# Performance work log

Hardware: AMD Instinct MI355X
Metric: run time of the kernel (lower is better)

## Reference

```python
import jax, jax.numpy as jnp
import numpy as np

B, T, D, E, H = 4, 2048, 2048, 4, 8192  # H = 4*D
TOPK = 2
CAPACITY_FACTOR = 1


def setup_inputs() -> dict:
    key = jax.random.key(0)
    k0, k1, k2, k3 = jax.random.split(key, 4)
    x = jax.random.normal(k0, (B, T, D), dtype=jnp.float32)
    Wg = jax.random.normal(k1, (D, E), dtype=jnp.float32) * 0.02  # router gate weight
    bg = jnp.zeros((E,), dtype=jnp.float32)                        # router gate bias (nn.Linear default)
    W1 = jax.random.normal(k2, (E, D, H), dtype=jnp.float32) * (1.0 / np.sqrt(D))  # per-expert fc (no bias)
    W2 = jax.random.normal(k3, (E, H, D), dtype=jnp.float32) * (1.0 / np.sqrt(H))  # per-expert proj (no bias)
    return {"x": x, "Wg": Wg, "bg": bg, "W1": W1, "W2": W2}


def reference(x, Wg, bg, W1, W2):
    Bq, Tq, Dq = x.shape
    N = Bq * Tq
    capacity = int(N * CAPACITY_FACTOR / E)  # static python int

    flat_x = x.reshape(N, Dq)
    logits = flat_x @ Wg + bg                              # [N, E]
    top_vals, top_idx = jax.lax.top_k(logits, TOPK)        # [N, TOPK]
    sparse = jnp.full_like(logits, -jnp.inf)
    sparse = sparse.at[jnp.arange(N)[:, None], top_idx].set(top_vals)
    probs = jax.nn.softmax(sparse, axis=-1)                # zeros outside top-k

    out = jnp.zeros_like(flat_x)
    for i in range(E):  # small fixed expert count
        assigned = (top_idx == i).any(axis=-1)             # [N]
        score = jnp.where(assigned, probs[:, i], -jnp.inf)
        sel_p, sel_idx = jax.lax.top_k(score, capacity)    # capacity-limited, highest prob first
        p = jnp.where(jnp.isfinite(sel_p), sel_p, 0.0)[:, None]  # invalid slots contribute 0
        tok = flat_x[sel_idx]                              # [cap, D]
        h = jax.nn.gelu(tok @ W1[i], approximate=False)    # exact GELU like nn.GELU()
        y = (h @ W2[i]) * p                                # [cap, D]
        out = out.at[sel_idx].add(y)
    return out.reshape(Bq, Tq, Dq)
```

## Files before the change

kernel.cpp:

```cpp
#include <hip/hip_runtime.h>
#include <hip/hip_bf16.h>
#include <math.h>
#include <stdint.h>

#define N_TOK 8192
#define DMODEL 2048
#define NEXP 4
#define HDIM 8192
#define CAP 2048

typedef __attribute__((ext_vector_type(4))) float f32x4;
typedef __attribute__((ext_vector_type(8))) short s16x8;
typedef __attribute__((ext_vector_type(4))) unsigned short u16x4;

__device__ __forceinline__ unsigned short f2bf(float f) {
  __hip_bfloat16 h = __float2bfloat16(f);
  return __builtin_bit_cast(unsigned short, h);
}

__device__ __forceinline__ void gload_lds16(const void* g, void* l) {
  __builtin_amdgcn_global_load_lds(
      (const __attribute__((address_space(1))) unsigned int*)(uintptr_t)g,
      (__attribute__((address_space(3))) unsigned int*)(unsigned int)(uintptr_t)l,
      16, 0, 0);
}

__global__ __launch_bounds__(256) void router_kernel(
    const float* __restrict__ x, const float* __restrict__ Wg,
    const float* __restrict__ bg, float* __restrict__ probs) {
  int token = blockIdx.x * 4 + (threadIdx.x >> 6);
  int lane = threadIdx.x & 63;
  const float* xr = x + (size_t)token * DMODEL;
  double a0 = 0, a1 = 0, a2 = 0, a3 = 0;
  for (int i = lane; i < DMODEL; i += 64) {
    float xv = xr[i];
    float4 w = ((const float4*)Wg)[i];
    a0 += (double)xv * (double)w.x;
    a1 += (double)xv * (double)w.y;
    a2 += (double)xv * (double)w.z;
    a3 += (double)xv * (double)w.w;
  }
  for (int off = 32; off > 0; off >>= 1) {
    a0 += __shfl_down(a0, off);
    a1 += __shfl_down(a1, off);
    a2 += __shfl_down(a2, off);
    a3 += __shfl_down(a3, off);
  }
  if (lane == 0) {
    float l[4] = {(float)(a0 + (double)bg[0]), (float)(a1 + (double)bg[1]),
                  (float)(a2 + (double)bg[2]), (float)(a3 + (double)bg[3])};
    int e1 = 0;
    for (int e = 1; e < 4; ++e) if (l[e] > l[e1]) e1 = e;
    int e2 = (e1 == 0) ? 1 : 0;
    for (int e = e2 + 1; e < 4; ++e) { if (e == e1) continue; if (l[e] > l[e2]) e2 = e; }
    float d = l[e2] - l[e1];
    float ex = expf(d);
    float z = 1.0f + ex;
    float pr[4] = {0.f, 0.f, 0.f, 0.f};
    pr[e1] = 1.0f / z;
    pr[e2] = ex / z;
    float* pp = probs + (size_t)token * 4;
    pp[0] = pr[0]; pp[1] = pr[1]; pp[2] = pr[2]; pp[3] = pr[3];
  }
}

__global__ __launch_bounds__(256) void select_kernel(
    const float* __restrict__ probs, int* __restrict__ sel_idx, float* __restrict__ sel_p) {
  __shared__ unsigned long long keys[N_TOK];
  int e = blockIdx.x;
  for (int i = threadIdx.x; i < N_TOK; i += blockDim.x) {
    float p = probs[(size_t)i * 4 + e];
    unsigned hi = (p > 0.f) ? __float_as_uint(p) : 0u;
    keys[i] = ((unsigned long long)hi << 32) | (unsigned)(0xFFFFFFFFu - (unsigned)i);
  }
  __syncthreads();
  for (int k = 2; k <= N_TOK; k <<= 1) {
    for (int j = k >> 1; j > 0; j >>= 1) {
      for (int i = threadIdx.x; i < N_TOK; i += blockDim.x) {
        int ixj = i ^ j;
        if (ixj > i) {
          bool ddd = ((i & k) == 0);
          unsigned long long a = keys[i], b = keys[ixj];
          if ((a < b) == ddd) { keys[i] = b; keys[ixj] = a; }
        }
      }
      __syncthreads();
    }
  }
  for (int c = threadIdx.x; c < CAP; c += blockDim.x) {
    unsigned long long kk = keys[c];
    unsigned idx = 0xFFFFFFFFu - (unsigned)(kk & 0xFFFFFFFFu);
    sel_idx[e * CAP + c] = (int)idx;
    sel_p[e * CAP + c] = __uint_as_float((unsigned)(kk >> 32));
  }
}

__global__ __launch_bounds__(256) void gather_kernel(
    const float* __restrict__ x, const int* __restrict__ sel_idx,
    unsigned short* __restrict__ tok) {
  int row = blockIdx.x;
  int t = sel_idx[row];
  const float4* src = (const float4*)(x + (size_t)t * DMODEL);
  u16x4* dst = (u16x4*)(tok + (size_t)row * DMODEL);
  for (int i = threadIdx.x; i < DMODEL / 4; i += blockDim.x) {
    float4 v = src[i];
    u16x4 w = {f2bf(v.x), f2bf(v.y), f2bf(v.z), f2bf(v.w)};
    dst[i] = w;
  }
}

__global__ __launch_bounds__(256) void transpose_convert_kernel(
    const float* __restrict__ W, unsigned short* __restrict__ WT, int K, int N) {
  __shared__ unsigned short tile[64][68];
  const size_t eoff = (size_t)blockIdx.z * (size_t)K * N;
  const float* Wp = W + eoff;
  unsigned short* Tp = WT + eoff;
  const int n0 = blockIdx.x * 64, k0 = blockIdx.y * 64;
  const int tid = threadIdx.x;
  const int nn4 = tid & 15, kk = tid >> 4;
#pragma unroll
  for (int p = 0; p < 4; ++p) {
    int k = kk + p * 16;
    float4 v = *(const float4*)&Wp[(size_t)(k0 + k) * N + n0 + nn4 * 4];
    tile[nn4 * 4 + 0][k] = f2bf(v.x);
    tile[nn4 * 4 + 1][k] = f2bf(v.y);
    tile[nn4 * 4 + 2][k] = f2bf(v.z);
    tile[nn4 * 4 + 3][k] = f2bf(v.w);
  }
  __syncthreads();
  const int nw = tid >> 4, cw = (tid & 15) * 4;
#pragma unroll
  for (int p = 0; p < 4; ++p) {
    int n = nw + p * 16;
    u16x4 v = *(const u16x4*)&tile[n][cw];
    *(u16x4*)&Tp[(size_t)(n0 + n) * K + k0 + cw] = v;
  }
}

template <int EPI>
__global__ __launch_bounds__(512) void gemm_kernel(
    const unsigned short* __restrict__ A, const unsigned short* __restrict__ Bt,
    void* __restrict__ C, const int* __restrict__ sel_idx, const float* __restrict__ sel_p,
    int M, int N, int K, size_t b_stride) {
  __shared__ unsigned short sh[65536];
  const int tid = threadIdx.x;
  const int lane = tid & 63;
  const int w = tid >> 6;
  const int wm = w >> 2, wn = w & 3;

  const int nwg = gridDim.x * gridDim.y;
  const int cpx = nwg >> 3;
  int linear = blockIdx.y * gridDim.x + blockIdx.x;
  linear = (linear & 7) * cpx + (linear >> 3);
  const int bx = linear & (gridDim.x - 1);
  const int by = linear >> __builtin_ctz(gridDim.x);
  const int m0 = by * 256, n0 = bx * 256;
  const unsigned short* Bp = Bt + (size_t)(m0 >> 11) * b_stride;

  f32x4 acc[8][4];
#pragma unroll
  for (int i = 0; i < 8; ++i)
#pragma unroll
    for (int j = 0; j < 4; ++j) acc[i][j] = (f32x4){0.f, 0.f, 0.f, 0.f};

  const int srow = w * 32 + (lane >> 3);
  const int schunk = ((lane & 7) ^ (lane >> 3)) * 8;
  const unsigned short* gA = A + (size_t)(m0 + srow) * K + schunk;
  const unsigned short* gB = Bp + (size_t)(n0 + srow) * K + schunk;
  const int ldsA = w * 2048;
  const int ldsB = 16384 + w * 2048;

  const int csw0 = (((lane >> 4) ^ (lane & 7)) << 3);
  const int arow = wm * 128 + (lane & 15);
  const int brow = wn * 64 + (lane & 15);

#pragma unroll
  for (int i = 0; i < 4; ++i) {
    gload_lds16(gA + (size_t)(i * 8) * K, &sh[ldsA + i * 512]);
    gload_lds16(gB + (size_t)(i * 8) * K, &sh[ldsB + i * 512]);
  }
  __syncthreads();

  int buf = 0;
  for (int kt = 0; kt < K; kt += 64, buf ^= 1) {
    const int nb = buf ^ 1;
    const unsigned short* shA = &sh[buf * 32768];
    const unsigned short* shB = &sh[buf * 32768 + 16384];
    const bool pf = (kt + 64) < K;
    if (pf) {
#pragma unroll
      for (int i = 0; i < 4; ++i)
        gload_lds16(gA + (size_t)(i * 8) * K + (kt + 64), &sh[nb * 32768 + ldsA + i * 512]);
    }
#pragma unroll
    for (int kb = 0; kb < 2; ++kb) {
      const int csw = csw0 ^ (kb << 5);
      s16x8 av[8], bv[4];
#pragma unroll
      for (int mf = 0; mf < 8; ++mf)
        av[mf] = *(const s16x8*)&shA[(arow + mf * 16) * 64 + csw];
#pragma unroll
      for (int nf = 0; nf < 4; ++nf)
        bv[nf] = *(const s16x8*)&shB[(brow + nf * 16) * 64 + csw];
      __builtin_amdgcn_s_setprio(1);
#pragma unroll
      for (int mf = 0; mf < 8; ++mf)
#pragma unroll
        for (int nf = 0; nf < 4; ++nf)
          acc[mf][nf] = __builtin_amdgcn_mfma_f32_16x16x32_bf16(av[mf], bv[nf], acc[mf][nf], 0, 0, 0);
      __builtin_amdgcn_s_setprio(0);
      if (kb == 0 && pf) {
#pragma unroll
        for (int i = 0; i < 4; ++i)
          gload_lds16(gB + (size_t)(i * 8) * K + (kt + 64), &sh[nb * 32768 + ldsB + i * 512]);
      }
    }
    __syncthreads();
  }

  if (EPI == 0) {
    unsigned short* Hc = (unsigned short*)C;
#pragma unroll
    for (int mf = 0; mf < 8; ++mf) {
      int rowb = m0 + wm * 128 + mf * 16 + ((lane >> 4) << 2);
#pragma unroll
      for (int nf = 0; nf < 4; ++nf) {
        int col = n0 + wn * 64 + nf * 16 + (lane & 15);
#pragma unroll
        for (int r = 0; r < 4; ++r) {
          float v = acc[mf][nf][r];
          float g = 0.5f * v * (1.0f + erff(v * 0.70710678118654752f));
          Hc[(size_t)(rowb + r) * N + col] = f2bf(g);
        }
      }
    }
  } else {
    float* O = (float*)C;
#pragma unroll
    for (int mf = 0; mf < 8; ++mf) {
      int rowb = m0 + wm * 128 + mf * 16 + ((lane >> 4) << 2);
      int tk[4];
      float pv[4];
#pragma unroll
      for (int r = 0; r < 4; ++r) { tk[r] = sel_idx[rowb + r]; pv[r] = sel_p[rowb + r]; }
#pragma unroll
      for (int nf = 0; nf < 4; ++nf) {
        int col = n0 + wn * 64 + nf * 16 + (lane & 15);
#pragma unroll
        for (int r = 0; r < 4; ++r)
          atomicAdd(&O[(size_t)tk[r] * DMODEL + col], acc[mf][nf][r] * pv[r]);
      }
    }
  }
}

extern "C" void kernel_launch(void* const* d_in, const int* in_sizes, int n_in,
                              void* d_out, int out_size, void* d_ws, size_t ws_size,
                              hipStream_t stream) {
  const float* x  = (const float*)d_in[0];
  const float* Wg = (const float*)d_in[1];
  const float* bg = (const float*)d_in[2];
  const float* W1 = (const float*)d_in[3];
  const float* W2 = (const float*)d_in[4];
  float* out = (float*)d_out;

  char* ws = (char*)d_ws;
  float* probs   = (float*)ws;
  int*   sel_idx = (int*)(ws + 131072);
  float* sel_p   = (float*)(ws + 131072 + 32768);
  unsigned short* tok = (unsigned short*)(ws + 196608);
  const size_t tok_b = (size_t)N_TOK * DMODEL * 2;
  const size_t h_b   = (size_t)N_TOK * HDIM * 2;
  const size_t w_b   = (size_t)NEXP * DMODEL * HDIM * 2;
  const size_t base  = 196608 + tok_b;

  hipMemsetAsync(d_out, 0, (size_t)out_size * sizeof(float), stream);
  router_kernel<<<N_TOK / 4, 256, 0, stream>>>(x, Wg, bg, probs);
  select_kernel<<<NEXP, 256, 0, stream>>>(probs, sel_idx, sel_p);
  gather_kernel<<<NEXP * CAP, 256, 0, stream>>>(x, sel_idx, tok);

  if (ws_size >= base + h_b + 2 * w_b) {
    unsigned short* h   = (unsigned short*)(ws + base);
    unsigned short* W1T = (unsigned short*)(ws + base + h_b);
    unsigned short* W2T = (unsigned short*)(ws + base + h_b + w_b);
    transpose_convert_kernel<<<dim3(HDIM / 64, DMODEL / 64, NEXP), 256, 0, stream>>>(
        W1, W1T, DMODEL, HDIM);
    transpose_convert_kernel<<<dim3(DMODEL / 64, HDIM / 64, NEXP), 256, 0, stream>>>(
        W2, W2T, HDIM, DMODEL);
    gemm_kernel<0><<<dim3(HDIM / 256, N_TOK / 256), 512, 0, stream>>>(
        tok, W1T, h, nullptr, nullptr, N_TOK, HDIM, DMODEL, (size_t)DMODEL * HDIM);
    gemm_kernel<1><<<dim3(DMODEL / 256, N_TOK / 256), 512, 0, stream>>>(
        h, W2T, out, sel_idx, sel_p, N_TOK, DMODEL, HDIM, (size_t)DMODEL * HDIM);
  } else {
    unsigned short* h    = (unsigned short*)(ws + base);
    unsigned short* wbuf = (unsigned short*)(ws + base + (size_t)CAP * HDIM * 2);
    for (int e = 0; e < NEXP; ++e) {
      transpose_convert_kernel<<<dim3(HDIM / 64, DMODEL / 64, 1), 256, 0, stream>>>(
          W1 + (size_t)e * DMODEL * HDIM, wbuf, DMODEL, HDIM);
      gemm_kernel<0><<<dim3(HDIM / 256, CAP / 256), 512, 0, stream>>>(
          tok + (size_t)e * CAP * DMODEL, wbuf, h, nullptr, nullptr, CAP, HDIM, DMODEL, 0);
      transpose_convert_kernel<<<dim3(DMODEL / 64, HDIM / 64, 1), 256, 0, stream>>>(
          W2 + (size_t)e * HDIM * DMODEL, wbuf, HDIM, DMODEL);
      gemm_kernel<1><<<dim3(DMODEL / 256, CAP / 256), 512, 0, stream>>>(
          h, wbuf, out, sel_idx + e * CAP, sel_p + e * CAP, CAP, DMODEL, HDIM, 0);
    }
  }
}
```

Before: 1.060 ms.

## Replace single-block bitonic sort with parallel rank-counting selection

The per-expert top-capacity selection previously ran a full bitonic sort of 8192 keys inside one block per expert, which is a long serial chain of barriers on only four blocks. It is replaced by a rank-by-counting kernel spread over many blocks: each thread counts how many keys beat its own and writes itself to that slot if the rank is within capacity. The router now writes the packed sort keys directly, and the workspace layout grows to hold them. This uses O(N^2) comparisons per expert, but they run across the whole GPU instead of a few blocks.

```diff
diff --git a/kernel.cpp b/kernel.cpp
--- a/kernel.cpp
+++ b/kernel.cpp
@@ -27,7 +27,7 @@
 
 __global__ __launch_bounds__(256) void router_kernel(
     const float* __restrict__ x, const float* __restrict__ Wg,
-    const float* __restrict__ bg, float* __restrict__ probs) {
+    const float* __restrict__ bg, unsigned long long* __restrict__ keys) {
   int token = blockIdx.x * 4 + (threadIdx.x >> 6);
   int lane = threadIdx.x & 63;
   const float* xr = x + (size_t)token * DMODEL;
@@ -56,42 +56,37 @@
     float d = l[e2] - l[e1];
     float ex = expf(d);
     float z = 1.0f + ex;
-    float pr[4] = {0.f, 0.f, 0.f, 0.f};
-    pr[e1] = 1.0f / z;
-    pr[e2] = ex / z;
-    float* pp = probs + (size_t)token * 4;
-    pp[0] = pr[0]; pp[1] = pr[1]; pp[2] = pr[2]; pp[3] = pr[3];
-  }
-}
-
-__global__ __launch_bounds__(256) void select_kernel(
-    const float* __restrict__ probs, int* __restrict__ sel_idx, float* __restrict__ sel_p) {
-  __shared__ unsigned long long keys[N_TOK];
-  int e = blockIdx.x;
-  for (int i = threadIdx.x; i < N_TOK; i += blockDim.x) {
-    float p = probs[(size_t)i * 4 + e];
-    unsigned hi = (p > 0.f) ? __float_as_uint(p) : 0u;
-    keys[i] = ((unsigned long long)hi << 32) | (unsigned)(0xFFFFFFFFu - (unsigned)i);
-  }
-  __syncthreads();
-  for (int k = 2; k <= N_TOK; k <<= 1) {
-    for (int j = k >> 1; j > 0; j >>= 1) {
-      for (int i = threadIdx.x; i < N_TOK; i += blockDim.x) {
-        int ixj = i ^ j;
-        if (ixj > i) {
-          bool ddd = ((i & k) == 0);
-          unsigned long long a = keys[i], b = keys[ixj];
-          if ((a < b) == ddd) { keys[i] = b; keys[ixj] = a; }
-        }
-      }
-      __syncthreads();
-    }
-  }
-  for (int c = threadIdx.x; c < CAP; c += blockDim.x) {
-    unsigned long long kk = keys[c];
-    unsigned idx = 0xFFFFFFFFu - (unsigned)(kk & 0xFFFFFFFFu);
-    sel_idx[e * CAP + c] = (int)idx;
-    sel_p[e * CAP + c] = __uint_as_float((unsigned)(kk >> 32));
+    float p1 = 1.0f / z, p2 = ex / z;
+    unsigned lo = 0xFFFFFFFFu - (unsigned)token;
+    for (int e = 0; e < 4; ++e) {
+      unsigned hi = (e == e1) ? __float_as_uint(p1) : (e == e2) ? __float_as_uint(p2) : 0u;
+      keys[(size_t)e * N_TOK + token] = ((unsigned long long)hi << 32) | lo;
+    }
+  }
+}
+
+__global__ __launch_bounds__(256) void rank_select_kernel(
+    const unsigned long long* __restrict__ keys, int* __restrict__ sel_idx,
+    float* __restrict__ sel_p) {
+  __shared__ unsigned long long kbuf[2048];
+  const int e = blockIdx.y;
+  const int i = blockIdx.x * 256 + threadIdx.x;
+  const unsigned long long my = keys[(size_t)e * N_TOK + i];
+  int rank = 0;
+  for (int c = 0; c < N_TOK; c += 2048) {
+    __syncthreads();
+    for (int j = threadIdx.x; j < 2048; j += 256)
+      kbuf[j] = keys[(size_t)e * N_TOK + c + j];
+    __syncthreads();
+#pragma unroll 8
+    for (int j = 0; j < 2048; j += 2) {
+      unsigned long long k0 = kbuf[j], k1 = kbuf[j + 1];
+      rank += (k0 > my) + (k1 > my);
+    }
+  }
+  if (rank < CAP) {
+    sel_idx[e * CAP + rank] = i;
+    sel_p[e * CAP + rank] = __uint_as_float((unsigned)(my >> 32));
   }
 }
 
@@ -265,18 +260,18 @@
   float* out = (float*)d_out;
 
   char* ws = (char*)d_ws;
-  float* probs   = (float*)ws;
-  int*   sel_idx = (int*)(ws + 131072);
-  float* sel_p   = (float*)(ws + 131072 + 32768);
-  unsigned short* tok = (unsigned short*)(ws + 196608);
+  unsigned long long* keys = (unsigned long long*)ws;
+  int*   sel_idx = (int*)(ws + 262144);
+  float* sel_p   = (float*)(ws + 262144 + 32768);
+  unsigned short* tok = (unsigned short*)(ws + 327680);
   const size_t tok_b = (size_t)N_TOK * DMODEL * 2;
   const size_t h_b   = (size_t)N_TOK * HDIM * 2;
   const size_t w_b   = (size_t)NEXP * DMODEL * HDIM * 2;
-  const size_t base  = 196608 + tok_b;
+  const size_t base  = 327680 + tok_b;
 
   hipMemsetAsync(d_out, 0, (size_t)out_size * sizeof(float), stream);
-  router_kernel<<<N_TOK / 4, 256, 0, stream>>>(x, Wg, bg, probs);
-  select_kernel<<<NEXP, 256, 0, stream>>>(probs, sel_idx, sel_p);
+  router_kernel<<<N_TOK / 4, 256, 0, stream>>>(x, Wg, bg, keys);
+  rank_select_kernel<<<dim3(N_TOK / 256, NEXP), 256, 0, stream>>>(keys, sel_idx, sel_p);
   gather_kernel<<<NEXP * CAP, 256, 0, stream>>>(x, sel_idx, tok);
 
   if (ws_size >= base + h_b + 2 * w_b) {
```

Result: faster. 867.7 us (-18.1%).
